# Optimization experiments

Hardware: AMD Instinct MI355X
Metric: run time of the kernel (lower is better)

## Reference

```python
import jax, jax.numpy as jnp
import numpy as np

N, C_IN, C_OUT, P, W, H = 32, 32, 16, 4, 16, 16
D = P * P
EPS = 1e-6


def squash(s, axis=-1):
    # v = ||s||^2/(1+||s||^2) * s/||s||, eps-stabilized as in the repo (eps=1e-6)
    n2 = jnp.sum(s * s, axis=axis, keepdims=True)
    n = jnp.sqrt(n2)
    return (n2 / (1.0 + n2)) * s / (n + EPS)


def setup_inputs() -> dict:
    key = jax.random.key(0)
    k1, k2, k3 = jax.random.split(key, 3)
    l = jax.random.normal(k1, (N, C_IN, D, W, H), jnp.float32)
    g = jax.random.normal(k2, (N, C_OUT, D), jnp.float32)
    weight = jax.random.normal(k3, (1, C_IN, 1, C_OUT, P, P), jnp.float32)
    return {"l": l, "g": g, "weight": weight, "num_iters": 3}


def reference(l, g, weight, num_iters):
    n, c, d, w, h = l.shape
    p = weight.shape[-1]
    c_out = weight.shape[3]
    # (N, C, D, W, H) -> (N, C, W*H, P, P)
    lp = jnp.transpose(l, (0, 1, 3, 4, 2)).reshape(n, c, w * h, p, p)
    # votes: pose matmul against per-(in,out) transform matrices
    # v[n,c,s,o] = lp[n,c,s] @ weight[0,c,0,o]   -> (N, C, WH, C_out, P, P)
    v = jnp.einsum('ncsij,cojk->ncsoik', lp, weight[0, :, 0])
    M = c * w * h
    v = v.reshape(n, M, c_out, d)          # (N, M, C_out, D)
    g = g[:, None, :, :]                    # (N, 1, C_out, D)
    # dynamic routing, logits initialized from agreement with the prior global capsule g
    b = jnp.sum(v * g, axis=-1, keepdims=True)   # (N, M, C_out, 1)
    cc = None
    for _ in range(num_iters):
        cc = jax.nn.softmax(b, axis=1)           # attention over input votes M
        g = squash(jnp.sum(cc * v, axis=1, keepdims=True))  # (N, 1, C_out, D)
        b = b + jnp.sum(v * g, axis=-1, keepdims=True)
    a = jnp.squeeze(cc, -1)   # (N, M, C_out)
    g = jnp.squeeze(g, 1)     # (N, C_out, D)
    return a, g
```

## Files before the change

### kernel.cpp

```cpp
#include <hip/hip_runtime.h>
#include <math.h>

#define N_   32
#define CIN  32
#define COUT 16
#define D_   16
#define S_   256
#define M_   (CIN * S_)

#define LOG2E 1.4426950408889634f

#define PSTRIDE (18 * 16)

#define WS_PB0 0
#define WS_PB1 (N_ * CIN * PSTRIDE)
#define WS_G1  (2 * N_ * CIN * PSTRIDE)

#define SW(s) ((((s) & 3)) ^ (((s) >> 2) & 3))

__device__ __forceinline__ void stage_tile(const float* __restrict__ gsrc,
                                           float* ls, int tid) {
  const float4* src = (const float4*)gsrc;
#pragma unroll
  for (int j = 0; j < 4; j++) {
    int f = ((tid & 3) << 6) + (tid >> 2) + (j << 8);
    float4 val = src[f];
    int dd = f >> 6;
    int u  = f & 63;
    int chunk = dd >> 2, lo = dd & 3;
    float vv[4] = {val.x, val.y, val.z, val.w};
#pragma unroll
    for (int m = 0; m < 4; m++) {
      int s = (u << 2) + m;
      int p = chunk ^ SW(s);
      ls[(s << 4) + (p << 2) + lo] = vv[m];
    }
  }
}

__device__ __forceinline__ void read_lp(const float* ls, int s, float* lp) {
  const float4* row = (const float4*)(ls + (s << 4));
  int sw = SW(s);
#pragma unroll
  for (int c = 0; c < 4; c++) {
    float4 q = row[c ^ sw];
    lp[c * 4 + 0] = q.x; lp[c * 4 + 1] = q.y;
    lp[c * 4 + 2] = q.z; lp[c * 4 + 3] = q.w;
  }
}

__device__ __forceinline__ float dot16(const float* a, const float* b) {
  float a0 = 0.f, a1 = 0.f, a2 = 0.f, a3 = 0.f;
#pragma unroll
  for (int k = 0; k < 4; k++) {
    a0 = fmaf(a[k],      b[k],      a0);
    a1 = fmaf(a[4 + k],  b[4 + k],  a1);
    a2 = fmaf(a[8 + k],  b[8 + k],  a2);
    a3 = fmaf(a[12 + k], b[12 + k], a3);
  }
  return (a0 + a1) + (a2 + a3);
}

__global__ __launch_bounds__(256, 2) void pass_kernel(
    const float* __restrict__ l, const float* __restrict__ wgt,
    const float* __restrict__ gprev, const float* __restrict__ part_in,
    float* __restrict__ gstore, float* __restrict__ part_out,
    float* __restrict__ edump, int mode) {
  const int bid = blockIdx.x;
  const int n = bid >> 5;
  const int c = bid & 31;
  const int tid = threadIdx.x;
  const int o = tid & 15;
  const int strip = tid >> 4;

  __shared__ float ls[D_ * S_];
  __shared__ float red[4][18][16];
  __shared__ float red2[18][16];

  stage_tile(l + ((size_t)(n * CIN + c)) * D_ * S_, ls, tid);

  float Greg[16];
  {
    const float4* gp = (const float4*)(gprev + (n * COUT + o) * 16);
#pragma unroll
    for (int i = 0; i < 4; i++) {
      float4 u = gp[i];
      Greg[i * 4 + 0] = u.x; Greg[i * 4 + 1] = u.y;
      Greg[i * 4 + 2] = u.z; Greg[i * 4 + 3] = u.w;
    }
  }

  float shift = 0.f;
  if (mode) {
    float H[18];
    const float* pn = part_in + (size_t)n * CIN * PSTRIDE + o;
    const int s45 = (tid >> 4) & 3;
    {
      const float* b0 = pn + (size_t)s45 * PSTRIDE;
#pragma unroll
      for (int f = 0; f < 18; f++) H[f] = b0[f * 16];
    }
#pragma unroll
    for (int q = 1; q < 8; q++) {
      const float* bq = pn + (size_t)(s45 + 4 * q) * PSTRIDE;
#pragma unroll
      for (int f = 0; f < 17; f++) H[f] += bq[f * 16];
      H[17] = fmaxf(H[17], bq[17 * 16]);
    }
#pragma unroll
    for (int off = 16; off <= 32; off <<= 1) {
#pragma unroll
      for (int f = 0; f < 17; f++) H[f] += __shfl_xor(H[f], off);
      H[17] = fmaxf(H[17], __shfl_xor(H[17], off));
    }
    float inv = 1.0f / H[16], n2 = 0.f, Sg[16];
#pragma unroll
    for (int d = 0; d < 16; d++) { Sg[d] = H[d] * inv; n2 = fmaf(Sg[d], Sg[d], n2); }
    float coef = n2 / ((1.f + n2) * (sqrtf(n2) + 1e-6f));
#pragma unroll
    for (int d = 0; d < 16; d++) Greg[d] = fmaf(coef, Sg[d], Greg[d]);
    shift = H[17];
    if (mode == 1 && c == 0 && tid < 16) {
      float* gs = gstore + (n * COUT + tid) * 16;
#pragma unroll
      for (int d = 0; d < 16; d++) gs[d] = Greg[d];
    }
  }

  float WG[16];
  {
    float wreg[16];
    const float4* wp = (const float4*)(wgt + (c * COUT + o) * 16);
#pragma unroll
    for (int i = 0; i < 4; i++) {
      float4 t = wp[i];
      wreg[i * 4 + 0] = t.x; wreg[i * 4 + 1] = t.y;
      wreg[i * 4 + 2] = t.z; wreg[i * 4 + 3] = t.w;
    }
#pragma unroll
    for (int i = 0; i < 4; i++)
#pragma unroll
      for (int j = 0; j < 4; j++) {
        float acc = 0.f;
#pragma unroll
        for (int k = 0; k < 4; k++)
          acc = fmaf(wreg[j * 4 + k], Greg[i * 4 + k], acc);
        WG[i * 4 + j] = acc * LOG2E;
      }
  }

  __syncthreads();

  float se = 0.f, bmx = -INFINITY, E[16];
#pragma unroll
  for (int d = 0; d < 16; d++) E[d] = 0.f;

#pragma unroll 4
  for (int it = 0; it < 16; it++) {
    float lp[16];
    read_lp(ls, strip + (it << 4), lp);
    float b = dot16(lp, WG) - shift;
    float e = exp2f(b);
    if (mode == 2) {
      edump[((size_t)(n * M_ + c * S_ + strip + (it << 4))) * COUT + o] = e;
    }
    bmx = fmaxf(bmx, b);
    se += e;
#pragma unroll
    for (int d = 0; d < 16; d++) E[d] = fmaf(e, lp[d], E[d]);
  }

#pragma unroll
  for (int off = 16; off <= 32; off <<= 1) {
    se += __shfl_xor(se, off);
    bmx = fmaxf(bmx, __shfl_xor(bmx, off));
#pragma unroll
    for (int d = 0; d < 16; d++) E[d] += __shfl_xor(E[d], off);
  }

  const int w = tid >> 6;
  if ((tid & 63) < 16) {
#pragma unroll
    for (int d = 0; d < 16; d++) red[w][d][o] = E[d];
    red[w][16][o] = se;
    red[w][17][o] = bmx;
  }
  __syncthreads();

  for (int p = tid; p < 288; p += 256) {
    int f = p >> 4, oo = p & 15;
    float v0 = red[0][f][oo], v1 = red[1][f][oo];
    float v2 = red[2][f][oo], v3 = red[3][f][oo];
    red2[f][oo] = (f == 17) ? fmaxf(fmaxf(v0, v1), fmaxf(v2, v3))
                            : ((v0 + v1) + (v2 + v3));
  }
  __syncthreads();

  if (tid < 16) {
    float wt[16];
    const float4* wp = (const float4*)(wgt + (c * COUT + tid) * 16);
#pragma unroll
    for (int i = 0; i < 4; i++) {
      float4 t = wp[i];
      wt[i * 4 + 0] = t.x; wt[i * 4 + 1] = t.y;
      wt[i * 4 + 2] = t.z; wt[i * 4 + 3] = t.w;
    }
    float Et[16];
#pragma unroll
    for (int d = 0; d < 16; d++) Et[d] = red2[d][tid];
    float set = red2[16][tid];
    float bmt = red2[17][tid];
    float* p0 = part_out + (size_t)(n * CIN + c) * PSTRIDE + tid;
#pragma unroll
    for (int i = 0; i < 4; i++)
#pragma unroll
      for (int k = 0; k < 4; k++) {
        float acc = 0.f;
#pragma unroll
        for (int j = 0; j < 4; j++) acc = fmaf(Et[i * 4 + j], wt[j * 4 + k], acc);
        p0[(i * 4 + k) * 16] = acc;
      }
    p0[16 * 16] = set;
    p0[17 * 16] = bmt + shift;
  }
}

__global__ __launch_bounds__(256, 2) void a_kernel(
    const float* __restrict__ part, float* __restrict__ a_out,
    float* __restrict__ g_out) {
  const int bid = blockIdx.x;
  const int n = bid >> 6;
  const int chunk = bid & 63;
  const int tid = threadIdx.x;

  __shared__ float sinv[16];

  if (tid < 16) {
    const float* pn = part + (size_t)n * CIN * PSTRIDE + tid;
    float se = 0.f;
    if (chunk == 0) {
      float S[16];
#pragma unroll
      for (int d = 0; d < 16; d++) S[d] = 0.f;
#pragma unroll 4
      for (int c = 0; c < CIN; c++) {
        const float* b = pn + (size_t)c * PSTRIDE;
#pragma unroll
        for (int f = 0; f < 16; f++) S[f] += b[f * 16];
        se += b[256];
      }
      float inv = 1.0f / se, n2 = 0.f;
#pragma unroll
      for (int d = 0; d < 16; d++) { S[d] *= inv; n2 = fmaf(S[d], S[d], n2); }
      float coef = n2 / ((1.f + n2) * (sqrtf(n2) + 1e-6f));
      float* go = g_out + (n * COUT + tid) * 16;
#pragma unroll
      for (int d = 0; d < 16; d++) go[d] = coef * S[d];
      sinv[tid] = inv;
    } else {
#pragma unroll 8
      for (int c = 0; c < CIN; c++) se += pn[(size_t)c * PSTRIDE + 256];
      sinv[tid] = 1.0f / se;
    }
  }
  __syncthreads();

  float4* pv = (float4*)(a_out + (size_t)n * (M_ * COUT) + (size_t)chunk * 2048);
#pragma unroll
  for (int r = 0; r < 2; r++) {
    int i4 = tid + (r << 8);
    int o0 = (i4 & 3) << 2;
    float4 v = pv[i4];
    v.x *= sinv[o0 + 0];
    v.y *= sinv[o0 + 1];
    v.z *= sinv[o0 + 2];
    v.w *= sinv[o0 + 3];
    pv[i4] = v;
  }
}

extern "C" void kernel_launch(void* const* d_in, const int* in_sizes, int n_in,
                              void* d_out, int out_size, void* d_ws, size_t ws_size,
                              hipStream_t stream) {
  const float* l = (const float*)d_in[0];
  const float* g = (const float*)d_in[1];
  const float* w = (const float*)d_in[2];

  float* out = (float*)d_out;
  float* ws = (float*)d_ws;
  float* a_out = out;
  float* g_out = out + (size_t)N_ * M_ * COUT;

  float* PB0 = ws + WS_PB0;
  float* PB1 = ws + WS_PB1;
  float* G1  = ws + WS_G1;

  pass_kernel<<<N_ * CIN, 256, 0, stream>>>(l, w, g, nullptr, nullptr, PB0,
                                            nullptr, 0);
  pass_kernel<<<N_ * CIN, 256, 0, stream>>>(l, w, g, PB0, G1, PB1,
                                            nullptr, 1);
  pass_kernel<<<N_ * CIN, 256, 0, stream>>>(l, w, G1, PB1, nullptr, PB0,
                                            a_out, 2);
  a_kernel<<<N_ * 64, 256, 0, stream>>>(PB0, a_out, g_out);
}
```

Before: 128.6 us.

## Use per-output row layout for partials and reduce routing state once per block

Changes the partial-sum buffer from a field-major layout (stride 16 across features) to a per-(n,c,o) row of 20 floats, so partials are written and read with float4 vector accesses. The reduction of previous-pass partials and the squash now run on only the first 64 threads into shared memory, and the results are broadcast to all threads through LDS. Previously every thread redundantly reduced 32 partial rows. It also raises the launch-bounds occupancy hints, which may pressure registers or cause spills.

Result: faster. 119.8 us (-6.8%).

```diff
diff --git a/kernel.cpp b/kernel.cpp
--- a/kernel.cpp
+++ b/kernel.cpp
@@ -10,11 +10,12 @@
 
 #define LOG2E 1.4426950408889634f
 
-#define PSTRIDE (18 * 16)
+#define PROW 20
+#define PIDX(n, c, o) ((((size_t)(n) * CIN + (c)) * COUT + (o)) * PROW)
 
 #define WS_PB0 0
-#define WS_PB1 (N_ * CIN * PSTRIDE)
-#define WS_G1  (2 * N_ * CIN * PSTRIDE)
+#define WS_PB1 (N_ * CIN * COUT * PROW)
+#define WS_G1  (2 * N_ * CIN * COUT * PROW)
 
 #define SW(s) ((((s) & 3)) ^ (((s) >> 2) & 3))
 
@@ -61,7 +62,7 @@
   return (a0 + a1) + (a2 + a3);
 }
 
-__global__ __launch_bounds__(256, 2) void pass_kernel(
+__global__ __launch_bounds__(256, 3) void pass_kernel(
     const float* __restrict__ l, const float* __restrict__ wgt,
     const float* __restrict__ gprev, const float* __restrict__ part_in,
     float* __restrict__ gstore, float* __restrict__ part_out,
@@ -76,6 +77,46 @@
   __shared__ float ls[D_ * S_];
   __shared__ float red[4][18][16];
   __shared__ float red2[18][16];
+  __shared__ float hd[16][20];
+
+  if (mode && tid < 64) {
+    const int ho = tid & 15, hs = tid >> 4;
+    float H[18];
+#pragma unroll
+    for (int f = 0; f < 17; f++) H[f] = 0.f;
+    H[17] = -INFINITY;
+#pragma unroll 2
+    for (int q = 0; q < 8; q++) {
+      const float* r = part_in + PIDX(n, hs + 4 * q, ho);
+      const float4* r4 = (const float4*)r;
+#pragma unroll
+      for (int i = 0; i < 4; i++) {
+        float4 v = r4[i];
+        H[i * 4 + 0] += v.x; H[i * 4 + 1] += v.y;
+        H[i * 4 + 2] += v.z; H[i * 4 + 3] += v.w;
+      }
+      H[16] += r[16];
+      H[17] = fmaxf(H[17], r[17]);
+    }
+#pragma unroll
+    for (int off = 16; off <= 32; off <<= 1) {
+#pragma unroll
+      for (int f = 0; f < 17; f++) H[f] += __shfl_xor(H[f], off);
+      H[17] = fmaxf(H[17], __shfl_xor(H[17], off));
+    }
+    if (tid < 16) {
+      float inv = 1.0f / H[16], n2 = 0.f, Sg[16];
+#pragma unroll
+      for (int d = 0; d < 16; d++) { Sg[d] = H[d] * inv; n2 = fmaf(Sg[d], Sg[d], n2); }
+      float coef = n2 / ((1.f + n2) * (sqrtf(n2) + 1e-6f));
+      float4* hq = (float4*)hd[tid];
+#pragma unroll
+      for (int i = 0; i < 4; i++)
+        hq[i] = make_float4(coef * Sg[i * 4 + 0], coef * Sg[i * 4 + 1],
+                            coef * Sg[i * 4 + 2], coef * Sg[i * 4 + 3]);
+      hd[tid][16] = H[17];
+    }
+  }
 
   stage_tile(l + ((size_t)(n * CIN + c)) * D_ * S_, ls, tid);
 
@@ -90,40 +131,28 @@
     }
   }
 
+  __syncthreads();
+
   float shift = 0.f;
   if (mode) {
-    float H[18];
-    const float* pn = part_in + (size_t)n * CIN * PSTRIDE + o;
-    const int s45 = (tid >> 4) & 3;
-    {
-      const float* b0 = pn + (size_t)s45 * PSTRIDE;
-#pragma unroll
-      for (int f = 0; f < 18; f++) H[f] = b0[f * 16];
-    }
-#pragma unroll
-    for (int q = 1; q < 8; q++) {
-      const float* bq = pn + (size_t)(s45 + 4 * q) * PSTRIDE;
-#pragma unroll
-      for (int f = 0; f < 17; f++) H[f] += bq[f * 16];
-      H[17] = fmaxf(H[17], bq[17 * 16]);
-    }
-#pragma unroll
-    for (int off = 16; off <= 32; off <<= 1) {
-#pragma unroll
-      for (int f = 0; f < 17; f++) H[f] += __shfl_xor(H[f], off);
-      H[17] = fmaxf(H[17], __shfl_xor(H[17], off));
-    }
-    float inv = 1.0f / H[16], n2 = 0.f, Sg[16];
-#pragma unroll
-    for (int d = 0; d < 16; d++) { Sg[d] = H[d] * inv; n2 = fmaf(Sg[d], Sg[d], n2); }
-    float coef = n2 / ((1.f + n2) * (sqrtf(n2) + 1e-6f));
-#pragma unroll
-    for (int d = 0; d < 16; d++) Greg[d] = fmaf(coef, Sg[d], Greg[d]);
-    shift = H[17];
+    const float4* hq = (const float4*)hd[o];
+#pragma unroll
+    for (int i = 0; i < 4; i++) {
+      float4 v = hq[i];
+      Greg[i * 4 + 0] += v.x; Greg[i * 4 + 1] += v.y;
+      Greg[i * 4 + 2] += v.z; Greg[i * 4 + 3] += v.w;
+    }
+    shift = hd[o][16];
     if (mode == 1 && c == 0 && tid < 16) {
       float* gs = gstore + (n * COUT + tid) * 16;
-#pragma unroll
-      for (int d = 0; d < 16; d++) gs[d] = Greg[d];
+      const float4* hp = (const float4*)hd[tid];
+      const float4* gp = (const float4*)(gprev + (n * COUT + tid) * 16);
+      float4* g4 = (float4*)gs;
+#pragma unroll
+      for (int i = 0; i < 4; i++) {
+        float4 a = gp[i], b = hp[i];
+        g4[i] = make_float4(a.x + b.x, a.y + b.y, a.z + b.z, a.w + b.w);
+      }
     }
   }
 
@@ -148,8 +177,6 @@
         WG[i * 4 + j] = acc * LOG2E;
       }
   }
-
-  __syncthreads();
 
   float se = 0.f, bmx = -INFINITY, E[16];
 #pragma unroll
@@ -208,24 +235,26 @@
     float Et[16];
 #pragma unroll
     for (int d = 0; d < 16; d++) Et[d] = red2[d][tid];
-    float set = red2[16][tid];
-    float bmt = red2[17][tid];
-    float* p0 = part_out + (size_t)(n * CIN + c) * PSTRIDE + tid;
-#pragma unroll
-    for (int i = 0; i < 4; i++)
-#pragma unroll
-      for (int k = 0; k < 4; k++) {
-        float acc = 0.f;
-#pragma unroll
-        for (int j = 0; j < 4; j++) acc = fmaf(Et[i * 4 + j], wt[j * 4 + k], acc);
-        p0[(i * 4 + k) * 16] = acc;
-      }
-    p0[16 * 16] = set;
-    p0[17 * 16] = bmt + shift;
-  }
-}
-
-__global__ __launch_bounds__(256, 2) void a_kernel(
+    float* p0 = part_out + PIDX(n, c, tid);
+    float4* p4 = (float4*)p0;
+#pragma unroll
+    for (int i = 0; i < 4; i++) {
+      float s0 = 0.f, s1 = 0.f, s2 = 0.f, s3 = 0.f;
+#pragma unroll
+      for (int j = 0; j < 4; j++) {
+        s0 = fmaf(Et[i * 4 + j], wt[j * 4 + 0], s0);
+        s1 = fmaf(Et[i * 4 + j], wt[j * 4 + 1], s1);
+        s2 = fmaf(Et[i * 4 + j], wt[j * 4 + 2], s2);
+        s3 = fmaf(Et[i * 4 + j], wt[j * 4 + 3], s3);
+      }
+      p4[i] = make_float4(s0, s1, s2, s3);
+    }
+    p0[16] = red2[16][tid];
+    p0[17] = red2[17][tid] + shift;
+  }
+}
+
+__global__ __launch_bounds__(256, 4) void a_kernel(
     const float* __restrict__ part, float* __restrict__ a_out,
     float* __restrict__ g_out) {
   const int bid = blockIdx.x;
@@ -236,7 +265,6 @@
   __shared__ float sinv[16];
 
   if (tid < 16) {
-    const float* pn = part + (size_t)n * CIN * PSTRIDE + tid;
     float se = 0.f;
     if (chunk == 0) {
       float S[16];
@@ -244,10 +272,15 @@
       for (int d = 0; d < 16; d++) S[d] = 0.f;
 #pragma unroll 4
       for (int c = 0; c < CIN; c++) {
-        const float* b = pn + (size_t)c * PSTRIDE;
-#pragma unroll
-        for (int f = 0; f < 16; f++) S[f] += b[f * 16];
-        se += b[256];
+        const float* r = part + PIDX(n, c, tid);
+        const float4* r4 = (const float4*)r;
+#pragma unroll
+        for (int i = 0; i < 4; i++) {
+          float4 v = r4[i];
+          S[i * 4 + 0] += v.x; S[i * 4 + 1] += v.y;
+          S[i * 4 + 2] += v.z; S[i * 4 + 3] += v.w;
+        }
+        se += r[16];
       }
       float inv = 1.0f / se, n2 = 0.f;
 #pragma unroll
@@ -259,7 +292,7 @@
       sinv[tid] = inv;
     } else {
 #pragma unroll 8
-      for (int c = 0; c < CIN; c++) se += pn[(size_t)c * PSTRIDE + 256];
+      for (int c = 0; c < CIN; c++) se += part[PIDX(n, c, tid) + 16];
       sinv[tid] = 1.0f / se;
     }
   }
```
